# Performance work log

Measured on AMD Instinct MI355X. Metric: run time of the kernel, lower is better.

## Reference

```python
import jax, jax.numpy as jnp
import numpy as np

H = 256  # hidden_size
IN = 256  # input_size
OUT = 128  # output_size


def _gru_cell(x, h, Wx, bx, Wh, bh):
    # x: (B, in), h: (B, H); Wx: (3H, in), Wh: (3H, H)
    xt = x @ Wx.T + bx  # (B, 3H)
    ht = h @ Wh.T + bh  # (B, 3H)
    xr, xz, xn = jnp.split(xt, 3, axis=1)
    hr, hz, hn = jnp.split(ht, 3, axis=1)
    r = jax.nn.sigmoid(xr + hr)
    z = jax.nn.sigmoid(xz + hz)
    n = jnp.tanh(xn + r * hn)
    return z * h + (1.0 - z) * n


def setup_inputs() -> dict:
    key = jax.random.key(0)
    ks = jax.random.split(key, 12)
    std = 1.0 / np.sqrt(H)
    u = lambda k, shape: jax.random.uniform(k, shape, jnp.float32, -std, std)
    return {
        "x": jax.random.normal(ks[0], (128, 1024, IN), jnp.float32),
        "Wx0": u(ks[1], (3 * H, IN)), "bx0": u(ks[2], (3 * H,)),
        "Wh0": u(ks[3], (3 * H, H)), "bh0": u(ks[4], (3 * H,)),
        "Wx1": u(ks[5], (3 * H, H)), "bx1": u(ks[6], (3 * H,)),
        "Wh1": u(ks[7], (3 * H, H)), "bh1": u(ks[8], (3 * H,)),
        "Wo": u(ks[9], (OUT, H)), "bo": u(ks[10], (OUT,)),
    }


def reference(x, Wx0, bx0, Wh0, bh0, Wx1, bx1, Wh1, bh1, Wo, bo):
    B = x.shape[0]
    h_init = (jnp.zeros((B, H), x.dtype), jnp.zeros((B, H), x.dtype))

    def step(carry, x_t):
        h0, h1 = carry
        h0 = _gru_cell(x_t, h0, Wx0, bx0, Wh0, bh0)
        h1 = _gru_cell(h0, h1, Wx1, bx1, Wh1, bh1)
        return (h0, h1), None

    # scan over time: x transposed to (T, B, in)
    (h0, h1), _ = jax.lax.scan(step, h_init, jnp.swapaxes(x, 0, 1))
    return h1 @ Wo.T + bo
```

## Files before the change

### kernel.cpp

```cpp
#include <hip/hip_runtime.h>
#include <stdint.h>


#define NPAIR 64

#define XR0_OFF 0
#define XR1_OFF 262144
#define HR0_OFF 524288
#define CTR_OFF 655360
#define FLG_OFF 659456

#if defined(__has_builtin)
#if __has_builtin(__builtin_amdgcn_fdot2)
#define USE_DOT2 1
#endif
#endif

typedef uint32_t u32x16 __attribute__((ext_vector_type(16)));
typedef _Float16 h2_t __attribute__((ext_vector_type(2)));
union H2U { uint32_t u; h2_t h; };
union FU  { uint32_t u; float f; };

__device__ __forceinline__ float bf2f(uint16_t b){ FU v; v.u=(uint32_t)b<<16; return v.f; }
__device__ __forceinline__ uint16_t f2bf(float f){
    FU v; v.f=f; uint32_t r=v.u+0x7fffu+((v.u>>16)&1u); return (uint16_t)(r>>16);
}
__device__ __forceinline__ float sigmoid_f(float x){ return 1.0f/(1.0f+__expf(-x)); }
__device__ __forceinline__ float tanh_f(float x){
    float ax=fabsf(x); float e=__expf(-2.0f*ax);
    float t=(1.0f-e)/(1.0f+e); return x<0.0f?-t:t;
}
__device__ __forceinline__ float dot2acc(uint32_t w, uint32_t v, float acc){
#ifdef USE_DOT2
    H2U a,b; a.u=w; b.u=v;
    return __builtin_amdgcn_fdot2(a.h, b.h, acc, false);
#else
    FU x0,x1,y0,y1;
    x0.u=w<<16; x1.u=w&0xffff0000u; y0.u=v<<16; y1.u=v&0xffff0000u;
    acc=fmaf(x0.f,y0.f,acc); return fmaf(x1.f,y1.f,acc);
#endif
}
__device__ __forceinline__ uint32_t cvt_bfpair(uint32_t raw){
#ifdef USE_DOT2
    FU lo,hi; lo.u=raw<<16; hi.u=raw&0xffff0000u;
    H2U r; r.h[0]=(_Float16)lo.f; r.h[1]=(_Float16)hi.f; return r.u;
#else
    return raw;
#endif
}
__device__ __forceinline__ uint32_t packpair(float lo, float hi){
#ifdef USE_DOT2
    H2U r; r.h[0]=(_Float16)lo; r.h[1]=(_Float16)hi; return r.u;
#else
    return (uint32_t)f2bf(lo) | ((uint32_t)f2bf(hi)<<16);
#endif
}
__device__ __forceinline__ u32x16 load16_bf(const uint4* p){
    uint4 a=p[0], b=p[1], c=p[2], d=p[3];
    u32x16 v;
    v[0]=cvt_bfpair(a.x);  v[1]=cvt_bfpair(a.y);  v[2]=cvt_bfpair(a.z);  v[3]=cvt_bfpair(a.w);
    v[4]=cvt_bfpair(b.x);  v[5]=cvt_bfpair(b.y);  v[6]=cvt_bfpair(b.z);  v[7]=cvt_bfpair(b.w);
    v[8]=cvt_bfpair(c.x);  v[9]=cvt_bfpair(c.y);  v[10]=cvt_bfpair(c.z); v[11]=cvt_bfpair(c.w);
    v[12]=cvt_bfpair(d.x); v[13]=cvt_bfpair(d.y); v[14]=cvt_bfpair(d.z); v[15]=cvt_bfpair(d.w);
    return v;
}
__device__ __forceinline__ u32x16 load16_f32(const float2* p){
    u32x16 v;
#define LF(i) v[i] = packpair(p[i].x, p[i].y)
    LF(0);LF(1);LF(2);LF(3);LF(4);LF(5);LF(6);LF(7);
    LF(8);LF(9);LF(10);LF(11);LF(12);LF(13);LF(14);LF(15);
#undef LF
    return v;
}

#define RLX_LD(p)    __hip_atomic_load((p),        __ATOMIC_RELAXED, __HIP_MEMORY_SCOPE_AGENT)
#define RLX_ST(p,v)  __hip_atomic_store((p), (v),  __ATOMIC_RELAXED, __HIP_MEMORY_SCOPE_AGENT)
__device__ __forceinline__ uint64_t RLX_LD64(const uint64_t* p){
    return __hip_atomic_load(p, __ATOMIC_RELAXED, __HIP_MEMORY_SCOPE_AGENT);
}
__device__ __forceinline__ void RLX_ST64(uint64_t* p, uint64_t v){
    __hip_atomic_store(p, v, __ATOMIC_RELAXED, __HIP_MEMORY_SCOPE_AGENT);
}

#define DOT16(WR, WZ, WN, G)                                                      \
    _Pragma("unroll")                                                             \
    for (int q = 0; q < 4; ++q) {                                                 \
        uint4 va = pa[4*(G)+q], vb = pb[4*(G)+q];                                 \
        ar0 = dot2acc(WR[4*q+0], va.x, ar0); ar1 = dot2acc(WR[4*q+0], vb.x, ar1); \
        az0 = dot2acc(WZ[4*q+0], va.x, az0); az1 = dot2acc(WZ[4*q+0], vb.x, az1); \
        an0 = dot2acc(WN[4*q+0], va.x, an0); an1 = dot2acc(WN[4*q+0], vb.x, an1); \
        ar0 = dot2acc(WR[4*q+1], va.y, ar0); ar1 = dot2acc(WR[4*q+1], vb.y, ar1); \
        az0 = dot2acc(WZ[4*q+1], va.y, az0); az1 = dot2acc(WZ[4*q+1], vb.y, az1); \
        an0 = dot2acc(WN[4*q+1], va.y, an0); an1 = dot2acc(WN[4*q+1], vb.y, an1); \
        ar0 = dot2acc(WR[4*q+2], va.z, ar0); ar1 = dot2acc(WR[4*q+2], vb.z, ar1); \
        az0 = dot2acc(WZ[4*q+2], va.z, az0); az1 = dot2acc(WZ[4*q+2], vb.z, az1); \
        an0 = dot2acc(WN[4*q+2], va.z, an0); an1 = dot2acc(WN[4*q+2], vb.z, an1); \
        ar0 = dot2acc(WR[4*q+3], va.w, ar0); ar1 = dot2acc(WR[4*q+3], vb.w, ar1); \
        az0 = dot2acc(WZ[4*q+3], va.w, az0); az1 = dot2acc(WZ[4*q+3], vb.w, az1); \
        an0 = dot2acc(WN[4*q+3], va.w, an0); an1 = dot2acc(WN[4*q+3], vb.w, an1); \
    }

__global__ void probe_init(const uint32_t* __restrict__ w,
                           uint32_t* __restrict__ ctr,
                           uint32_t* __restrict__ flag) {
    int i = threadIdx.x;
    for (int k = i; k < 4096; k += 1024) ctr[k] = 0u;
    if (i == 0) {
        int c = 0;
        for (int j = 0; j < 64; ++j) {
            uint32_t e = (w[j] >> 7) & 0xFFu;
            c += (e >= 0x60u && e <= 0x7Cu) ? 1 : 0;
        }
        flag[0] = (c >= 32) ? 1u : 0u;
    }
}

__global__ void __launch_bounds__(512) __attribute__((amdgpu_waves_per_eu(2, 2)))
gru7(const void* __restrict__ xin,
     const void* __restrict__ Wx0, const void* __restrict__ bx0,
     const void* __restrict__ Wh0, const void* __restrict__ bh0,
     const void* __restrict__ Wx1, const void* __restrict__ bx1,
     const void* __restrict__ Wh1, const void* __restrict__ bh1,
     const void* __restrict__ Wo,  const void* __restrict__ bo,
     void* __restrict__ out,
     uint32_t* __restrict__ ws)
{
    const int tid  = threadIdx.x;
    const int pair = blockIdx.x & (NPAIR - 1);
    const int role = blockIdx.x >> 6;
    const int p    = tid >> 1;
    const int hs   = tid & 1;

    uint64_t* XR0p = (uint64_t*)(ws + XR0_OFF) + pair * 2048;
    uint64_t* XR1p = (uint64_t*)(ws + XR1_OFF) + pair * 2048;
    uint64_t* HRp  = (uint64_t*)(ws + HR0_OFF) + pair * 1024;
    uint32_t* CTR  = ws + CTR_OFF;
    const int isbf = (int)ws[FLG_OFF];

    uint32_t* myprg   = CTR + role * 1024 + pair * 16;
    uint32_t* consprg = CTR + (role + 1) * 1024 + pair * 16;

    const void* Wsel; const void* bsel;
    if      (role == 0) { Wsel = Wx0; bsel = bx0; }
    else if (role == 1) { Wsel = Wh0; bsel = bh0; }
    else if (role == 2) { Wsel = Wx1; bsel = bx1; }
    else                { Wsel = Wh1; bsel = bh1; }

    u32x16 wr0,wr1,wr2,wr3, wz0,wz1,wz2,wz3, wn0,wn1,wn2,wn3;
    float br, bz, bn;
    if (isbf) {
        const uint4* W4 = (const uint4*)Wsel;
        const uint4* r0 = W4 + (size_t)p * 32 + hs * 16;
        const uint4* r1 = W4 + (size_t)(p + 256) * 32 + hs * 16;
        const uint4* r2 = W4 + (size_t)(p + 512) * 32 + hs * 16;
        wr0=load16_bf(r0);    wr1=load16_bf(r0+4);  wr2=load16_bf(r0+8);  wr3=load16_bf(r0+12);
        wz0=load16_bf(r1);    wz1=load16_bf(r1+4);  wz2=load16_bf(r1+8);  wz3=load16_bf(r1+12);
        wn0=load16_bf(r2);    wn1=load16_bf(r2+4);  wn2=load16_bf(r2+8);  wn3=load16_bf(r2+12);
        const uint16_t* bs = (const uint16_t*)bsel;
        br = bf2f(bs[p]); bz = bf2f(bs[p+256]); bn = bf2f(bs[p+512]);
    } else {
        const float2* W2 = (const float2*)Wsel;
        const float2* r0 = W2 + (size_t)p * 128 + hs * 64;
        const float2* r1 = W2 + (size_t)(p + 256) * 128 + hs * 64;
        const float2* r2 = W2 + (size_t)(p + 512) * 128 + hs * 64;
        wr0=load16_f32(r0);    wr1=load16_f32(r0+16); wr2=load16_f32(r0+32); wr3=load16_f32(r0+48);
        wz0=load16_f32(r1);    wz1=load16_f32(r1+16); wz2=load16_f32(r1+32); wz3=load16_f32(r1+48);
        wn0=load16_f32(r2);    wn1=load16_f32(r2+16); wn2=load16_f32(r2+32); wn3=load16_f32(r2+48);
        const float* bs = (const float*)bsel;
        br = bs[p]; bz = bs[p+256]; bn = bs[p+512];
    }

    __shared__ __align__(16) uint32_t sb[544];

    if (role == 0 || role == 2) {
        const uint32_t* xs32 = (const uint32_t*)xin;
        const float2*   xsf  = (const float2*)xin;
        const int bglob = pair * 2 + (tid >> 7);
        const int i128  = tid & 127;
        const int spos  = (tid >> 7) * 136 + i128 + ((i128 >> 6) << 2);
        uint32_t xpref = 0;
        uint2 pfh; pfh.x = 0; pfh.y = 0;
        if (role == 0 && tid < 256) {
            if (isbf) xpref = cvt_bfpair(xs32[(size_t)bglob * 131072 + i128]);
            else { float2 f = xsf[(size_t)bglob * 131072 + i128]; xpref = packpair(f.x, f.y); }
        }
        uint64_t* outring = (role == 0) ? XR0p : XR1p;
        uint32_t prog_seen = 0;

        for (int t = 0; t < 1024; ++t) {
            if (t >= 4 && prog_seen + 3 < (uint32_t)t) {
                do { prog_seen = RLX_LD(consprg);
                     if (prog_seen + 3 < (uint32_t)t) __builtin_amdgcn_s_sleep(2);
                } while (prog_seen + 3 < (uint32_t)t);
            }
            if (tid < 256) {
                uint32_t pk;
                if (role == 0) pk = xpref;
                else {
                    uint2 v = pfh;
                    const uint32_t want = (uint32_t)(t + 1);
                    if (v.y != want) {
                        const uint64_t* a = HRp + (t & 3) * 256 + tid;
                        uint64_t u;
                        do { u = RLX_LD64(a);
                             v.x = (uint32_t)u; v.y = (uint32_t)(u >> 32);
                             if (v.y != want) __builtin_amdgcn_s_sleep(1);
                        } while (v.y != want);
                    }
                    pk = v.x;
                }
                sb[(t & 1) * 272 + spos] = pk;
            }
            __syncthreads();
            if (tid == 0 && !(t & 1)) RLX_ST(myprg, (uint32_t)t);
            if (tid < 256 && t < 1023) {
                if (role == 0) {
                    if (isbf) xpref = cvt_bfpair(xs32[(size_t)bglob * 131072 + (t+1)*128 + i128]);
                    else { float2 f = xsf[(size_t)bglob * 131072 + (t+1)*128 + i128]; xpref = packpair(f.x, f.y); }
                } else {
                    uint64_t u = RLX_LD64(HRp + ((t + 1) & 3) * 256 + tid);
                    pfh.x = (uint32_t)u; pfh.y = (uint32_t)(u >> 32);
                }
            }
            float ar0=0,ar1=0,az0=0,az1=0,an0=0,an1=0;
            {
                const uint4* pa = ((const uint4*)&sb[(t & 1) * 272]) + hs * 17;
                const uint4* pb = pa + 34;
                DOT16(wr0,wz0,wn0,0); DOT16(wr1,wz1,wn1,1);
                DOT16(wr2,wz2,wn2,2); DOT16(wr3,wz3,wn3,3);
            }
            float R0 = ar0 + __shfl_xor(ar0,1), R1 = ar1 + __shfl_xor(ar1,1);
            float Z0 = az0 + __shfl_xor(az0,1), Z1 = az1 + __shfl_xor(az1,1);
            float N0 = an0 + __shfl_xor(an0,1), N1 = an1 + __shfl_xor(an1,1);
            float sr = (hs ? R1 : R0) + br;
            float sz = (hs ? Z1 : Z0) + bz;
            float sn = (hs ? N1 : N0) + bn;
            H2U lo; lo.h[0] = (_Float16)sr; lo.h[1] = (_Float16)sz;
            H2U sn16; sn16.u = 0; sn16.h[0] = (_Float16)sn;
            uint32_t hi = (sn16.u & 0xFFFFu) | (((uint32_t)(t + 1)) << 16);
            RLX_ST64(outring + (t & 3) * 512 + 2 * p + hs,
                     (uint64_t)lo.u | ((uint64_t)hi << 32));
        }
    } else {
        const uint64_t* xr64 = (role == 1) ? XR0p : XR1p;
        float h_reg = 0.0f;
        for (int i = tid; i < 544; i += 512) sb[i] = 0u;
        uint2 pfx; pfx.x = 0; pfx.y = 0;
        uint32_t prog_seen = 0;
        const int hj   = p >> 1;
        const int hpos = hs * 136 + hj + ((hj >> 6) << 2);

        for (int t = 0; t < 1024; ++t) {
            if (role == 1 && t >= 4 && prog_seen + 3 < (uint32_t)t) {
                do { prog_seen = RLX_LD(consprg);
                     if (prog_seen + 3 < (uint32_t)t) __builtin_amdgcn_s_sleep(2);
                } while (prog_seen + 3 < (uint32_t)t);
            }
            uint2 v = pfx;
            const uint32_t want = (uint32_t)(t + 1);
            if ((v.y >> 16) != want) {
                const uint64_t* a = xr64 + (t & 3) * 512 + 2 * p + hs;
                uint64_t u;
                do { u = RLX_LD64(a);
                     v.x = (uint32_t)u; v.y = (uint32_t)(u >> 32);
                     if ((v.y >> 16) != want) __builtin_amdgcn_s_sleep(1);
                } while ((v.y >> 16) != want);
            }
            H2U ua; ua.u = v.x;
            H2U ub; ub.u = v.y & 0xFFFFu;
            float xr = (float)ua.h[0], xz = (float)ua.h[1], xn = (float)ub.h[0];
            __syncthreads();
            if (tid == 0 && !(t & 1)) RLX_ST(myprg, (uint32_t)t);
            if (t < 1023) {
                uint64_t u = RLX_LD64(xr64 + ((t + 1) & 3) * 512 + 2 * p + hs);
                pfx.x = (uint32_t)u; pfx.y = (uint32_t)(u >> 32);
            }
            float ar0=0,ar1=0,az0=0,az1=0,an0=0,an1=0;
            {
                const uint4* pa = ((const uint4*)&sb[(t & 1) * 272]) + hs * 17;
                const uint4* pb = pa + 34;
                DOT16(wr0,wz0,wn0,0); DOT16(wr1,wz1,wn1,1);
                DOT16(wr2,wz2,wn2,2); DOT16(wr3,wz3,wn3,3);
            }
            float R0 = ar0 + __shfl_xor(ar0,1), R1 = ar1 + __shfl_xor(ar1,1);
            float Z0 = az0 + __shfl_xor(az0,1), Z1 = az1 + __shfl_xor(az1,1);
            float N0 = an0 + __shfl_xor(an0,1), N1 = an1 + __shfl_xor(an1,1);
            float r = sigmoid_f(xr + (hs ? R1 : R0) + br);
            float z = sigmoid_f(xz + (hs ? Z1 : Z0) + bz);
            float n = tanh_f(xn + r * ((hs ? N1 : N0) + bn));
            h_reg = z * h_reg + (1.0f - z) * n;
            float hp = __shfl_xor(h_reg, 2);
            if (!(tid & 2)) {
                uint32_t pk = packpair(h_reg, hp);
                sb[((t + 1) & 1) * 272 + hpos] = pk;
                if (role == 1)
                    RLX_ST64(HRp + (t & 3) * 256 + hs * 128 + hj,
                             (uint64_t)pk | ((uint64_t)(t + 1) << 32));
            }
        }
        __syncthreads();
        if (tid == 0) RLX_ST(myprg, 1024u);

        if (role == 3 && tid < 256) {
            const int j = tid >> 1, bb = tid & 1;
            const uint32_t* hv = &sb[bb * 136];
            float acc;
            if (isbf) {
                acc = bf2f(((const uint16_t*)bo)[j]);
                const uint32_t* wo = (const uint32_t*)Wo + j * 128;
#pragma unroll 8
                for (int c = 0; c < 128; ++c)
                    acc = dot2acc(cvt_bfpair(wo[c]), hv[c + ((c >> 6) << 2)], acc);
                ((uint16_t*)out)[(pair * 2 + bb) * 128 + j] = f2bf(acc);
            } else {
                acc = ((const float*)bo)[j];
                const float2* wo = (const float2*)Wo + j * 128;
#pragma unroll 8
                for (int c = 0; c < 128; ++c) {
                    float2 f = wo[c];
                    acc = dot2acc(packpair(f.x, f.y), hv[c + ((c >> 6) << 2)], acc);
                }
                ((float*)out)[(pair * 2 + bb) * 128 + j] = acc;
            }
        }
    }
}

extern "C" void kernel_launch(void* const* d_in, const int* in_sizes, int n_in,
                              void* d_out, int out_size, void* d_ws, size_t ws_size,
                              hipStream_t stream) {
    uint32_t* ws  = (uint32_t*)d_ws;
    uint32_t* CTR = ws + CTR_OFF;
    uint32_t* FLG = ws + FLG_OFF;

    probe_init<<<dim3(1), dim3(1024), 0, stream>>>((const uint32_t*)d_in[1], CTR, FLG);
    gru7<<<dim3(256), dim3(512), 0, stream>>>(
        d_in[0], d_in[1], d_in[2], d_in[3], d_in[4],
        d_in[5], d_in[6], d_in[7], d_in[8], d_in[9], d_in[10],
        d_out, ws);
}
```

Before: 2.720 ms.

## Split GRU dot products four ways across 1024-thread blocks with lighter barriers

Each output row's reduction dimension is now split across four threads instead of two, so every thread keeps half as many weight registers and does half the dot2 work per step; partial sums are combined with two xor shuffles. Blocks grow to 1024 threads and the shared-memory padding layout changes to match. __syncthreads is replaced with a raw LDS-wait plus s_barrier, and sigmoid/tanh use the hardware reciprocal instead of a division. The goal is a shorter per-timestep critical path in the serial recurrence, at the cost of extra shuffles and larger barriers.

Result: slower. 3.316 ms (+21.9%).

```diff
diff --git a/kernel.cpp b/kernel.cpp
--- a/kernel.cpp
+++ b/kernel.cpp
@@ -14,6 +14,9 @@
 #if __has_builtin(__builtin_amdgcn_fdot2)
 #define USE_DOT2 1
 #endif
+#if __has_builtin(__builtin_amdgcn_rcpf)
+#define USE_RCP 1
+#endif
 #endif
 
 typedef uint32_t u32x16 __attribute__((ext_vector_type(16)));
@@ -25,10 +28,17 @@
 __device__ __forceinline__ uint16_t f2bf(float f){
     FU v; v.f=f; uint32_t r=v.u+0x7fffu+((v.u>>16)&1u); return (uint16_t)(r>>16);
 }
-__device__ __forceinline__ float sigmoid_f(float x){ return 1.0f/(1.0f+__expf(-x)); }
+__device__ __forceinline__ float rcp_f(float x){
+#ifdef USE_RCP
+    return __builtin_amdgcn_rcpf(x);
+#else
+    return 1.0f/x;
+#endif
+}
+__device__ __forceinline__ float sigmoid_f(float x){ return rcp_f(1.0f+__expf(-x)); }
 __device__ __forceinline__ float tanh_f(float x){
     float ax=fabsf(x); float e=__expf(-2.0f*ax);
-    float t=(1.0f-e)/(1.0f+e); return x<0.0f?-t:t;
+    float t=(1.0f-e)*rcp_f(1.0f+e); return x<0.0f?-t:t;
 }
 __device__ __forceinline__ float dot2acc(uint32_t w, uint32_t v, float acc){
 #ifdef USE_DOT2
@@ -81,6 +91,12 @@
 __device__ __forceinline__ void RLX_ST64(uint64_t* p, uint64_t v){
     __hip_atomic_store(p, v, __ATOMIC_RELAXED, __HIP_MEMORY_SCOPE_AGENT);
 }
+
+#define BAR() do {                                              \
+    asm volatile("s_waitcnt lgkmcnt(0)" ::: "memory");          \
+    __builtin_amdgcn_s_barrier();                               \
+    asm volatile("" ::: "memory");                              \
+} while (0)
 
 #define DOT16(WR, WZ, WN, G)                                                      \
     _Pragma("unroll")                                                             \
@@ -115,8 +131,8 @@
     }
 }
 
-__global__ void __launch_bounds__(512) __attribute__((amdgpu_waves_per_eu(2, 2)))
-gru7(const void* __restrict__ xin,
+__global__ void __launch_bounds__(1024) __attribute__((amdgpu_waves_per_eu(4)))
+gru8(const void* __restrict__ xin,
      const void* __restrict__ Wx0, const void* __restrict__ bx0,
      const void* __restrict__ Wh0, const void* __restrict__ bh0,
      const void* __restrict__ Wx1, const void* __restrict__ bx1,
@@ -128,8 +144,8 @@
     const int tid  = threadIdx.x;
     const int pair = blockIdx.x & (NPAIR - 1);
     const int role = blockIdx.x >> 6;
-    const int p    = tid >> 1;
-    const int hs   = tid & 1;
+    const int p    = tid >> 2;
+    const int ks   = tid & 3;
 
     uint64_t* XR0p = (uint64_t*)(ws + XR0_OFF) + pair * 2048;
     uint64_t* XR1p = (uint64_t*)(ws + XR1_OFF) + pair * 2048;
@@ -146,38 +162,38 @@
     else if (role == 2) { Wsel = Wx1; bsel = bx1; }
     else                { Wsel = Wh1; bsel = bh1; }
 
-    u32x16 wr0,wr1,wr2,wr3, wz0,wz1,wz2,wz3, wn0,wn1,wn2,wn3;
+    u32x16 wr0,wr1, wz0,wz1, wn0,wn1;
     float br, bz, bn;
     if (isbf) {
         const uint4* W4 = (const uint4*)Wsel;
-        const uint4* r0 = W4 + (size_t)p * 32 + hs * 16;
-        const uint4* r1 = W4 + (size_t)(p + 256) * 32 + hs * 16;
-        const uint4* r2 = W4 + (size_t)(p + 512) * 32 + hs * 16;
-        wr0=load16_bf(r0);    wr1=load16_bf(r0+4);  wr2=load16_bf(r0+8);  wr3=load16_bf(r0+12);
-        wz0=load16_bf(r1);    wz1=load16_bf(r1+4);  wz2=load16_bf(r1+8);  wz3=load16_bf(r1+12);
-        wn0=load16_bf(r2);    wn1=load16_bf(r2+4);  wn2=load16_bf(r2+8);  wn3=load16_bf(r2+12);
+        const uint4* r0 = W4 + (size_t)p * 32 + ks * 8;
+        const uint4* r1 = W4 + (size_t)(p + 256) * 32 + ks * 8;
+        const uint4* r2 = W4 + (size_t)(p + 512) * 32 + ks * 8;
+        wr0=load16_bf(r0);   wr1=load16_bf(r0+4);
+        wz0=load16_bf(r1);   wz1=load16_bf(r1+4);
+        wn0=load16_bf(r2);   wn1=load16_bf(r2+4);
         const uint16_t* bs = (const uint16_t*)bsel;
         br = bf2f(bs[p]); bz = bf2f(bs[p+256]); bn = bf2f(bs[p+512]);
     } else {
         const float2* W2 = (const float2*)Wsel;
-        const float2* r0 = W2 + (size_t)p * 128 + hs * 64;
-        const float2* r1 = W2 + (size_t)(p + 256) * 128 + hs * 64;
-        const float2* r2 = W2 + (size_t)(p + 512) * 128 + hs * 64;
-        wr0=load16_f32(r0);    wr1=load16_f32(r0+16); wr2=load16_f32(r0+32); wr3=load16_f32(r0+48);
-        wz0=load16_f32(r1);    wz1=load16_f32(r1+16); wz2=load16_f32(r1+32); wz3=load16_f32(r1+48);
-        wn0=load16_f32(r2);    wn1=load16_f32(r2+16); wn2=load16_f32(r2+32); wn3=load16_f32(r2+48);
+        const float2* r0 = W2 + (size_t)p * 128 + ks * 32;
+        const float2* r1 = W2 + (size_t)(p + 256) * 128 + ks * 32;
+        const float2* r2 = W2 + (size_t)(p + 512) * 128 + ks * 32;
+        wr0=load16_f32(r0);   wr1=load16_f32(r0+16);
+        wz0=load16_f32(r1);   wz1=load16_f32(r1+16);
+        wn0=load16_f32(r2);   wn1=load16_f32(r2+16);
         const float* bs = (const float*)bsel;
         br = bs[p]; bz = bs[p+256]; bn = bs[p+512];
     }
 
-    __shared__ __align__(16) uint32_t sb[544];
+    __shared__ __align__(16) uint32_t sb[576];
 
     if (role == 0 || role == 2) {
         const uint32_t* xs32 = (const uint32_t*)xin;
         const float2*   xsf  = (const float2*)xin;
         const int bglob = pair * 2 + (tid >> 7);
         const int i128  = tid & 127;
-        const int spos  = (tid >> 7) * 136 + i128 + ((i128 >> 6) << 2);
+        const int spos  = (tid >> 7) * 144 + i128 + ((i128 >> 5) << 2);
         uint32_t xpref = 0;
         uint2 pfh; pfh.x = 0; pfh.y = 0;
         if (role == 0 && tid < 256) {
@@ -209,9 +225,9 @@
                     }
                     pk = v.x;
                 }
-                sb[(t & 1) * 272 + spos] = pk;
-            }
-            __syncthreads();
+                sb[(t & 1) * 288 + spos] = pk;
+            }
+            BAR();
             if (tid == 0 && !(t & 1)) RLX_ST(myprg, (uint32_t)t);
             if (tid < 256 && t < 1023) {
                 if (role == 0) {
@@ -224,31 +240,38 @@
             }
             float ar0=0,ar1=0,az0=0,az1=0,an0=0,an1=0;
             {
-                const uint4* pa = ((const uint4*)&sb[(t & 1) * 272]) + hs * 17;
-                const uint4* pb = pa + 34;
+                const uint4* pa = ((const uint4*)sb) + (t & 1) * 72 + ks * 9;
+                const uint4* pb = pa + 36;
                 DOT16(wr0,wz0,wn0,0); DOT16(wr1,wz1,wn1,1);
-                DOT16(wr2,wz2,wn2,2); DOT16(wr3,wz3,wn3,3);
-            }
-            float R0 = ar0 + __shfl_xor(ar0,1), R1 = ar1 + __shfl_xor(ar1,1);
-            float Z0 = az0 + __shfl_xor(az0,1), Z1 = az1 + __shfl_xor(az1,1);
-            float N0 = an0 + __shfl_xor(an0,1), N1 = an1 + __shfl_xor(an1,1);
-            float sr = (hs ? R1 : R0) + br;
-            float sz = (hs ? Z1 : Z0) + bz;
-            float sn = (hs ? N1 : N0) + bn;
-            H2U lo; lo.h[0] = (_Float16)sr; lo.h[1] = (_Float16)sz;
-            H2U sn16; sn16.u = 0; sn16.h[0] = (_Float16)sn;
-            uint32_t hi = (sn16.u & 0xFFFFu) | (((uint32_t)(t + 1)) << 16);
-            RLX_ST64(outring + (t & 3) * 512 + 2 * p + hs,
-                     (uint64_t)lo.u | ((uint64_t)hi << 32));
+            }
+            float s;
+            s = ar0 + __shfl_xor(ar0,1); float R0 = s + __shfl_xor(s,2);
+            s = ar1 + __shfl_xor(ar1,1); float R1 = s + __shfl_xor(s,2);
+            s = az0 + __shfl_xor(az0,1); float Z0 = s + __shfl_xor(s,2);
+            s = az1 + __shfl_xor(az1,1); float Z1 = s + __shfl_xor(s,2);
+            s = an0 + __shfl_xor(an0,1); float N0 = s + __shfl_xor(s,2);
+            s = an1 + __shfl_xor(an1,1); float N1 = s + __shfl_xor(s,2);
+            if (ks < 2) {
+                float sr = (ks ? R1 : R0) + br;
+                float sz = (ks ? Z1 : Z0) + bz;
+                float sn = (ks ? N1 : N0) + bn;
+                H2U lo; lo.h[0] = (_Float16)sr; lo.h[1] = (_Float16)sz;
+                H2U sn16; sn16.u = 0; sn16.h[0] = (_Float16)sn;
+                uint32_t hi = (sn16.u & 0xFFFFu) | (((uint32_t)(t + 1)) << 16);
+                RLX_ST64(outring + (t & 3) * 512 + 2 * p + ks,
+                         (uint64_t)lo.u | ((uint64_t)hi << 32));
+            }
         }
     } else {
         const uint64_t* xr64 = (role == 1) ? XR0p : XR1p;
         float h_reg = 0.0f;
-        for (int i = tid; i < 544; i += 512) sb[i] = 0u;
+        for (int i = tid; i < 576; i += 1024) sb[i] = 0u;
         uint2 pfx; pfx.x = 0; pfx.y = 0;
         uint32_t prog_seen = 0;
-        const int hj   = p >> 1;
-        const int hpos = hs * 136 + hj + ((hj >> 6) << 2);
+        const int b     = ks & 1;
+        const int hj    = tid >> 3;
+        const int hpos  = b * 144 + hj + ((hj >> 5) << 2);
+        const int wlane = !(tid & 6);
 
         for (int t = 0; t < 1024; ++t) {
             if (role == 1 && t >= 4 && prog_seen + 3 < (uint32_t)t) {
@@ -259,7 +282,7 @@
             uint2 v = pfx;
             const uint32_t want = (uint32_t)(t + 1);
             if ((v.y >> 16) != want) {
-                const uint64_t* a = xr64 + (t & 3) * 512 + 2 * p + hs;
+                const uint64_t* a = xr64 + (t & 3) * 512 + 2 * p + b;
                 uint64_t u;
                 do { u = RLX_LD64(a);
                      v.x = (uint32_t)u; v.y = (uint32_t)(u >> 32);
@@ -269,48 +292,51 @@
             H2U ua; ua.u = v.x;
             H2U ub; ub.u = v.y & 0xFFFFu;
             float xr = (float)ua.h[0], xz = (float)ua.h[1], xn = (float)ub.h[0];
-            __syncthreads();
+            BAR();
             if (tid == 0 && !(t & 1)) RLX_ST(myprg, (uint32_t)t);
             if (t < 1023) {
-                uint64_t u = RLX_LD64(xr64 + ((t + 1) & 3) * 512 + 2 * p + hs);
+                uint64_t u = RLX_LD64(xr64 + ((t + 1) & 3) * 512 + 2 * p + b);
                 pfx.x = (uint32_t)u; pfx.y = (uint32_t)(u >> 32);
             }
             float ar0=0,ar1=0,az0=0,az1=0,an0=0,an1=0;
             {
-                const uint4* pa = ((const uint4*)&sb[(t & 1) * 272]) + hs * 17;
-                const uint4* pb = pa + 34;
+                const uint4* pa = ((const uint4*)sb) + (t & 1) * 72 + ks * 9;
+                const uint4* pb = pa + 36;
                 DOT16(wr0,wz0,wn0,0); DOT16(wr1,wz1,wn1,1);
-                DOT16(wr2,wz2,wn2,2); DOT16(wr3,wz3,wn3,3);
-            }
-            float R0 = ar0 + __shfl_xor(ar0,1), R1 = ar1 + __shfl_xor(ar1,1);
-            float Z0 = az0 + __shfl_xor(az0,1), Z1 = az1 + __shfl_xor(az1,1);
-            float N0 = an0 + __shfl_xor(an0,1), N1 = an1 + __shfl_xor(an1,1);
-            float r = sigmoid_f(xr + (hs ? R1 : R0) + br);
-            float z = sigmoid_f(xz + (hs ? Z1 : Z0) + bz);
-            float n = tanh_f(xn + r * ((hs ? N1 : N0) + bn));
+            }
+            float s;
+            s = ar0 + __shfl_xor(ar0,1); float R0 = s + __shfl_xor(s,2);
+            s = ar1 + __shfl_xor(ar1,1); float R1 = s + __shfl_xor(s,2);
+            s = az0 + __shfl_xor(az0,1); float Z0 = s + __shfl_xor(s,2);
+            s = az1 + __shfl_xor(az1,1); float Z1 = s + __shfl_xor(s,2);
+            s = an0 + __shfl_xor(an0,1); float N0 = s + __shfl_xor(s,2);
+            s = an1 + __shfl_xor(an1,1); float N1 = s + __shfl_xor(s,2);
+            float r = sigmoid_f(xr + (b ? R1 : R0) + br);
+            float z = sigmoid_f(xz + (b ? Z1 : Z0) + bz);
+            float n = tanh_f(xn + r * ((b ? N1 : N0) + bn));
             h_reg = z * h_reg + (1.0f - z) * n;
-            float hp = __shfl_xor(h_reg, 2);
-            if (!(tid & 2)) {
+            float hp = __shfl_xor(h_reg, 4);
+            if (wlane) {
                 uint32_t pk = packpair(h_reg, hp);
-                sb[((t + 1) & 1) * 272 + hpos] = pk;
+                sb[((t + 1) & 1) * 288 + hpos] = pk;
                 if (role == 1)
-                    RLX_ST64(HRp + (t & 3) * 256 + hs * 128 + hj,
+                    RLX_ST64(HRp + (t & 3) * 256 + b * 128 + hj,
                              (uint64_t)pk | ((uint64_t)(t + 1) << 32));
             }
         }
-        __syncthreads();
+        BAR();
         if (tid == 0) RLX_ST(myprg, 1024u);
 
         if (role == 3 && tid < 256) {
             const int j = tid >> 1, bb = tid & 1;
-            const uint32_t* hv = &sb[bb * 136];
+            const uint32_t* hv = &sb[bb * 144];
             float acc;
             if (isbf) {
                 acc = bf2f(((const uint16_t*)bo)[j]);
                 const uint32_t* wo = (const uint32_t*)Wo + j * 128;
 #pragma unroll 8
                 for (int c = 0; c < 128; ++c)
-                    acc = dot2acc(cvt_bfpair(wo[c]), hv[c + ((c >> 6) << 2)], acc);
+                    acc = dot2acc(cvt_bfpair(wo[c]), hv[c + ((c >> 5) << 2)], acc);
                 ((uint16_t*)out)[(pair * 2 + bb) * 128 + j] = f2bf(acc);
             } else {
                 acc = ((const float*)bo)[j];
@@ -318,7 +344,7 @@
 #pragma unroll 8
                 for (int c = 0; c < 128; ++c) {
                     float2 f = wo[c];
-                    acc = dot2acc(packpair(f.x, f.y), hv[c + ((c >> 6) << 2)], acc);
+                    acc = dot2acc(packpair(f.x, f.y), hv[c + ((c >> 5) << 2)], acc);
                 }
                 ((float*)out)[(pair * 2 + bb) * 128 + j] = acc;
             }
@@ -334,7 +360,7 @@
     uint32_t* FLG = ws + FLG_OFF;
 
     probe_init<<<dim3(1), dim3(1024), 0, stream>>>((const uint32_t*)d_in[1], CTR, FLG);
-    gru7<<<dim3(256), dim3(512), 0, stream>>>(
+    gru8<<<dim3(256), dim3(1024), 0, stream>>>(
         d_in[0], d_in[1], d_in[2], d_in[3], d_in[4],
         d_in[5], d_in[6], d_in[7], d_in[8], d_in[9], d_in[10],
         d_out, ws);
```
